# Performance work log

Hardware: AMD Instinct MI355X
Metric: run time of the kernel (lower is better)

The kernel has to match this reference:

```python
import jax, jax.numpy as jnp
import numpy as np

B = 8192       # atmospheric columns (batch)
NLAY = 60      # vertical levels (RNN sequence length)
NX = 4         # per-level input features
NXS = 3        # surface scalar inputs
NH1 = 64       # rnn1 hidden
NH2 = 64       # rnn2 hidden
NMEM = 16      # latent memory width (nh_mem)
NY = 4         # per-level outputs
NYS = 3        # surface outputs


def _lstm(x, h0, c0, Wih, Whh, bih, bhh):
    """PyTorch-convention LSTM (gate order i,f,g,o). x: [B,T,nx] -> ([B,T,nh], hL, cL)."""
    b = bih + bhh
    WihT = Wih.T
    WhhT = Whh.T

    def step(carry, xt):
        h, c = carry
        g = xt @ WihT + h @ WhhT + b
        i, f, gg, o = jnp.split(g, 4, axis=-1)
        c = jax.nn.sigmoid(f) * c + jax.nn.sigmoid(i) * jnp.tanh(gg)
        h = jax.nn.sigmoid(o) * jnp.tanh(c)
        return (h, c), h

    (hL, cL), ys = jax.lax.scan(step, (h0, c0), jnp.swapaxes(x, 0, 1))
    return jnp.swapaxes(ys, 0, 1), hL, cL


def setup_inputs() -> dict:
    key = jax.random.key(0)
    ks = jax.random.split(key, 30)

    def p(i, shape):
        return jax.random.normal(ks[i], shape, jnp.float32) * 0.05

    return {
        "inputs_main": jax.random.normal(ks[0], (B, NLAY, NX), jnp.float32),
        "inputs_aux": jax.random.normal(ks[1], (B, NXS), jnp.float32),
        "rnn1_mem": jax.random.normal(ks[2], (B, NLAY, NMEM), jnp.float32),
        # mlp_initial: Linear(nx, nneur[0])
        "Wi": p(3, (NH1, NX)), "bi": p(4, (NH1,)),
        # mlp_surface1/2: Linear(nx_sfc, nh_rnn1)
        "Ws1": p(5, (NH1, NXS)), "bs1": p(6, (NH1,)),
        "Ws2": p(7, (NH1, NXS)), "bs2": p(8, (NH1,)),
        # mlp_toa1/2: Linear(1, nh_rnn2)
        "Wt1": p(9, (NH2, 1)), "bt1": p(10, (NH2,)),
        "Wt2": p(11, (NH2, 1)), "bt2": p(12, (NH2,)),
        # rnn1: LSTM(NH1+NMEM -> NH1)
        "Wih1": p(13, (4 * NH1, NH1 + NMEM)), "Whh1": p(14, (4 * NH1, NH1)),
        "bih1": p(15, (4 * NH1,)), "bhh1": p(16, (4 * NH1,)),
        # rnn2: LSTM(NH1 -> NH2)
        "Wih2": p(17, (4 * NH2, NH1)), "Whh2": p(18, (4 * NH2, NH2)),
        "bih2": p(19, (4 * NH2,)), "bhh2": p(20, (4 * NH2,)),
        # mlp_latent: Linear(NH2, NMEM)
        "Wl": p(21, (NMEM, NH2)), "bl": p(22, (NMEM,)),
        # mlp_output: Linear(NMEM, NY)
        "Wo": p(23, (NY, NMEM)), "bo": p(24, (NY,)),
        # mlp_surface_output: Linear(NH2, NYS)
        "Wso": p(25, (NYS, NH2)), "bso": p(26, (NYS,)),
    }


def reference(inputs_main, inputs_aux, rnn1_mem, Wi, bi, Ws1, bs1, Ws2, bs2,
              Wt1, bt1, Wt2, bt2, Wih1, Whh1, bih1, bhh1, Wih2, Whh2, bih2, bhh2,
              Wl, bl, Wo, bo, Wso, bso):
    # initial MLP + tanh
    x = jnp.tanh(inputs_main @ Wi.T + bi)                       # [B,L,NH1]
    # concat convective memory
    x = jnp.concatenate([x, rnn1_mem], axis=2)                  # [B,L,NH1+NMEM]
    # rnn1 runs surface->TOA: flip level axis
    x = jnp.flip(x, axis=1)
    hx = jnp.tanh(inputs_aux @ Ws1.T + bs1)                     # surface-conditioned h0
    cx = jnp.tanh(inputs_aux @ Ws2.T + bs2)
    r1, _, _ = _lstm(x, hx, cx, Wih1, Whh1, bih1, bhh1)
    r1 = jnp.flip(r1, axis=1)                                   # back to TOA->surface
    # rnn2 initialized from TOA scalar
    toa = inputs_aux[:, 1:2]
    hx2 = toa @ Wt1.T + bt1
    cx2 = toa @ Wt2.T + bt2
    r2, hL, _ = _lstm(r1, hx2, cx2, Wih2, Whh2, bih2, bhh2)     # [B,L,NH2]
    # intermediate latent MLP -> new per-level memory
    lat = r2 @ Wl.T + bl                                        # [B,L,NMEM]
    new_mem = lat
    out = lat @ Wo.T + bo                                       # [B,L,NY]
    out_sfc = hL @ Wso.T + bso                                  # [B,NYS]
    return (out, out_sfc, new_mem)
```

## Files before the change

kernel.cpp:

```cpp
#include <hip/hip_runtime.h>
#include <hip/hip_bf16.h>

#define BATCH 8192
#define NLAY  60
#define ROWS  16
#define TPB   256
#define SX    136
#define SM    968
#define SI    244
#define LOG2E 1.44269504089f
#define T2L   2.88539008178f

typedef unsigned short ushort_t;
typedef __attribute__((ext_vector_type(8))) short short8;
typedef __attribute__((ext_vector_type(4))) float f32x4;
typedef __attribute__((ext_vector_type(4))) float f4v;

__device__ __forceinline__ float rcp_(float x) { return __builtin_amdgcn_rcpf(x); }
__device__ __forceinline__ float ex2_(float x) { return __builtin_amdgcn_exp2f(x); }
__device__ __forceinline__ ushort_t f2bu(float f) {
  unsigned u = __float_as_uint(f);
  return (ushort_t)((u + 0x7FFFu + ((u >> 16) & 1u)) >> 16);
}
__device__ __forceinline__ unsigned pkbf(float a, float b) {
  union { __hip_bfloat162 h; unsigned u; } c;
  c.h = __float22bfloat162_rn(make_float2(a, b));
  return c.u;
}
__device__ __forceinline__ f32x4 mfma16(short8 a, short8 b, f32x4 c) {
  return __builtin_amdgcn_mfma_f32_16x16x32_bf16(a, b, c, 0, 0, 0);
}

__global__ void wtranspose(const float* __restrict__ Wih1, const float* __restrict__ Whh1,
                           const float* __restrict__ Wih2, const float* __restrict__ Whh2,
                           const float* __restrict__ Wl,   const float* __restrict__ Wo,
                           const float* __restrict__ Wso,  ushort_t* __restrict__ frag) {
  int e = blockIdx.x * 256 + threadIdx.x;
  float v;
  if (e < 40960) {
    int j = e & 7, lx = (e >> 3) & 63, rest = e >> 9;
    int ks = rest % 5, gw = rest / 5;
    int g = gw & 3, wv = gw >> 2;
    int row = g * 64 + wv * 16 + (lx & 15);
    int k = ks * 32 + (lx >> 4) * 8 + j;
    v = (k < 64)  ? Wih1[row * 80 + k]
      : (k < 128) ? Whh1[row * 64 + (k - 64)]
      : (k < 144) ? Wih1[row * 80 + 64 + (k - 128)]
      : 0.0f;
    v *= (g == 2) ? T2L : LOG2E;
  } else if (e < 73728) {
    int e2 = e - 40960;
    int j = e2 & 7, lx = (e2 >> 3) & 63, rest = e2 >> 9;
    int ks = rest & 3, g = (rest >> 2) & 3, wv = rest >> 4;
    int row = g * 64 + wv * 16 + (lx & 15);
    int k = ks * 32 + (lx >> 4) * 8 + j;
    v = (k < 64) ? Wih2[row * 64 + k] : Whh2[row * 64 + (k - 64)];
    v *= (g == 2) ? T2L : LOG2E;
  } else if (e < 74752) {
    int e3 = e - 73728;
    int j = e3 & 7, lx = (e3 >> 3) & 63, ks = e3 >> 9;
    int n = lx & 15, k = ks * 32 + (lx >> 4) * 8 + j;
    v = Wl[n * 64 + k];
  } else if (e < 75776) {
    int e4 = e - 74752;
    int j = e4 & 7, lx = (e4 >> 3) & 63, ks = e4 >> 9;
    int n = lx & 15, k = ks * 32 + (lx >> 4) * 8 + j;
    v = 0.0f;
    if (n < 4) {
#pragma unroll
      for (int m = 0; m < 16; ++m) v += Wo[n * 16 + m] * Wl[m * 64 + k];
    }
  } else {
    int e5 = e - 75776;
    int j = e5 & 7, lx = (e5 >> 3) & 63, ks = e5 >> 9;
    int n = lx & 15, k = ks * 32 + (lx >> 4) * 8 + j;
    v = (n < 3) ? Wso[n * 64 + k] : 0.0f;
  }
  frag[e] = f2bu(v);
}

__global__ __launch_bounds__(TPB, 2)
void lstm_fused(const float* __restrict__ inputs_main, const float* __restrict__ inputs_aux,
                const float* __restrict__ rnn1_mem,
                const float* __restrict__ Wi,  const float* __restrict__ bi,
                const float* __restrict__ Ws1, const float* __restrict__ bs1,
                const float* __restrict__ Ws2, const float* __restrict__ bs2,
                const float* __restrict__ Wt1, const float* __restrict__ bt1,
                const float* __restrict__ Wt2, const float* __restrict__ bt2,
                const float* __restrict__ bih1, const float* __restrict__ bhh1,
                const float* __restrict__ bih2, const float* __restrict__ bhh2,
                const float* __restrict__ bl,  const float* __restrict__ Wo,
                const float* __restrict__ bo,  const float* __restrict__ bso,
                const ushort_t* __restrict__ frag,
                ushort_t* __restrict__ r1buf,
                float* __restrict__ out, float* __restrict__ out_sfc,
                float* __restrict__ new_mem) {
  const ushort_t* W1f = frag;
  const ushort_t* W2f = frag + 40960;
  const ushort_t* WlF = frag + 73728;
  const ushort_t* WcF = frag + 74752;
  const ushort_t* WsF = frag + 75776;

  __shared__ __align__(16) ushort_t xh[2][16 * SX];
  __shared__ __align__(16) ushort_t memAll[16 * SM];
  __shared__ __align__(16) float    inm[16 * SI];

  const int tid = threadIdx.x;
  const int lane = tid & 63, w = tid >> 6;
  const int ln = lane & 15, lq = lane >> 4;
  const int u = w * 16 + ln;
  const int rowbase = lq * 4;
  const int b0 = blockIdx.x * ROWS;
  const int xr = tid >> 4, xm = tid & 15, xc0 = xm * 4;
  const int rr8 = tid >> 3, ch8 = tid & 7;

  ushort_t* r1blk = r1buf + (size_t)blockIdx.x * (60 * 16 * 64);

  short8 B1f[4][5];
#pragma unroll
  for (int g = 0; g < 4; ++g)
#pragma unroll
    for (int ks = 0; ks < 5; ++ks)
      B1f[g][ks] = *(const short8*)(W1f + (((w * 4 + g) * 5 + ks) << 9) + (lane << 3));
  float bg1[4];
#pragma unroll
  for (int g = 0; g < 4; ++g)
    bg1[g] = (bih1[g * 64 + u] + bhh1[g * 64 + u]) * ((g == 2) ? T2L : LOG2E);

  f4v wif[4];
#pragma unroll
  for (int cc = 0; cc < 4; ++cc) wif[cc] = *(const f4v*)(Wi + (xc0 + cc) * 4) * T2L;
  f4v bifv = *(const f4v*)(bi + xc0) * T2L;

  for (int e = tid; e < 16 * 240; e += TPB) {
    int r = e / 240, c = e - r * 240;
    inm[r * SI + c] = inputs_main[(size_t)(b0 + r) * 240 + c];
  }
  for (int e = tid; e < 16 * 960; e += TPB) {
    int r = e / 960, c = e - r * 960;
    memAll[r * SM + c] = f2bu(rnn1_mem[(size_t)(b0 + r) * 960 + c]);
  }
  __syncthreads();

  float ct1[4];
  {
    f4v xin = *(const f4v*)&inm[xr * SI + 59 * 4];
    float xp[4];
#pragma unroll
    for (int cc = 0; cc < 4; ++cc) {
      float a = fmaf(wif[cc][3], xin[3], fmaf(wif[cc][2], xin[2],
                fmaf(wif[cc][1], xin[1], fmaf(wif[cc][0], xin[0], bifv[cc]))));
      xp[cc] = fmaf(rcp_(1.0f + ex2_(a)), -2.0f, 1.0f);
    }
    *(uint2*)&xh[0][xr * SX + xc0] = make_uint2(pkbf(xp[0], xp[1]), pkbf(xp[2], xp[3]));

    float w10 = Ws1[u * 3 + 0] * T2L, w11 = Ws1[u * 3 + 1] * T2L, w12 = Ws1[u * 3 + 2] * T2L;
    float bb1 = bs1[u] * T2L;
    float w20 = Ws2[u * 3 + 0] * T2L, w21 = Ws2[u * 3 + 1] * T2L, w22 = Ws2[u * 3 + 2] * T2L;
    float bb2 = bs2[u] * T2L;
#pragma unroll
    for (int reg = 0; reg < 4; ++reg) {
      int row = rowbase + reg;
      const float* ax = inputs_aux + (size_t)(b0 + row) * 3;
      float a0 = ax[0], a1 = ax[1], a2 = ax[2];
      float ha = w10 * a0 + w11 * a1 + w12 * a2 + bb1;
      xh[0][row * SX + 64 + u] = f2bu(fmaf(rcp_(1.0f + ex2_(ha)), -2.0f, 1.0f));
      float ca = w20 * a0 + w21 * a1 + w22 * a2 + bb2;
      ct1[reg] = fmaf(rcp_(1.0f + ex2_(ca)), -2.0f * T2L, T2L);
    }
  }
  __syncthreads();

  ushort_t* r1t = r1blk + rowbase * 64 + u;
  unsigned sxv[4], syv[4];
  int pb = 0;

  for (int tg = 14; tg >= 0; --tg) {
#pragma unroll
    for (int s = 3; s >= 0; --s) {
      const int t = tg * 4 + s;
      const int nb = pb ^ 1;
      const ushort_t* xrow = &xh[pb][ln * SX];
      short8 af0 = *(const short8*)(xrow + lq * 8);
      short8 af1 = *(const short8*)(xrow + 32 + lq * 8);
      short8 af2 = *(const short8*)(xrow + 64 + lq * 8);
      short8 af3 = *(const short8*)(xrow + 96 + lq * 8);
      short8 af4 = {};
      if (lq < 2) af4 = *(const short8*)(memAll + ln * SM + t * 16 + lq * 8);

      f32x4 acc[4];
#pragma unroll
      for (int g = 0; g < 4; ++g) acc[g] = (f32x4){bg1[g], bg1[g], bg1[g], bg1[g]};
#pragma unroll
      for (int g = 0; g < 4; ++g) {
        acc[g] = mfma16(af0, B1f[g][0], acc[g]);
        acc[g] = mfma16(af1, B1f[g][1], acc[g]);
        acc[g] = mfma16(af2, B1f[g][2], acc[g]);
        acc[g] = mfma16(af3, B1f[g][3], acc[g]);
        acc[g] = mfma16(af4, B1f[g][4], acc[g]);
      }

      if (t > 0) {
        f4v xin = *(const f4v*)&inm[xr * SI + (t - 1) * 4];
        float xp[4];
#pragma unroll
        for (int cc = 0; cc < 4; ++cc) {
          float a = fmaf(wif[cc][3], xin[3], fmaf(wif[cc][2], xin[2],
                    fmaf(wif[cc][1], xin[1], fmaf(wif[cc][0], xin[0], bifv[cc]))));
          xp[cc] = fmaf(rcp_(1.0f + ex2_(a)), -2.0f, 1.0f);
        }
        *(uint2*)&xh[nb][xr * SX + xc0] = make_uint2(pkbf(xp[0], xp[1]), pkbf(xp[2], xp[3]));
      }

      float h[4];
#pragma unroll
      for (int reg = 0; reg < 4; ++reg) {
        float si = rcp_(1.0f + ex2_(-acc[0][reg]));
        float sf = rcp_(1.0f + ex2_(-acc[1][reg]));
        float so = rcp_(1.0f + ex2_(-acc[3][reg]));
        float gt = fmaf(rcp_(1.0f + ex2_(acc[2][reg])), -2.0f * T2L, T2L);
        ct1[reg] = fmaf(sf, ct1[reg], si * gt);
        float tc = fmaf(rcp_(1.0f + ex2_(ct1[reg])), -2.0f, 1.0f);
        h[reg] = so * tc;
      }
      unsigned h01 = pkbf(h[0], h[1]), h23 = pkbf(h[2], h[3]);
      sxv[s] = h01; syv[s] = h23;
      if (t > 0) {
        xh[nb][(rowbase + 0) * SX + 64 + u] = (ushort_t)h01;
        xh[nb][(rowbase + 1) * SX + 64 + u] = (ushort_t)(h01 >> 16);
        xh[nb][(rowbase + 2) * SX + 64 + u] = (ushort_t)h23;
        xh[nb][(rowbase + 3) * SX + 64 + u] = (ushort_t)(h23 >> 16);
      } else {
        xh[nb][(rowbase + 0) * SX + u] = (ushort_t)h01;
        xh[nb][(rowbase + 1) * SX + u] = (ushort_t)(h01 >> 16);
        xh[nb][(rowbase + 2) * SX + u] = (ushort_t)h23;
        xh[nb][(rowbase + 3) * SX + u] = (ushort_t)(h23 >> 16);
      }
      __syncthreads();
      pb = nb;
    }
    ushort_t* rp = r1t + (tg << 12);
#pragma unroll
    for (int s = 0; s < 4; ++s) {
      unsigned a = sxv[s], b = syv[s];
      rp[s * 1024 + 0 * 64] = (ushort_t)a;
      rp[s * 1024 + 1 * 64] = (ushort_t)(a >> 16);
      rp[s * 1024 + 2 * 64] = (ushort_t)b;
      rp[s * 1024 + 3 * 64] = (ushort_t)(b >> 16);
    }
  }

  short8 B2f[4][4];
#pragma unroll
  for (int g = 0; g < 4; ++g)
#pragma unroll
    for (int ks = 0; ks < 4; ++ks)
      B2f[g][ks] = *(const short8*)(W2f + (((w * 4 + g) * 4 + ks) << 9) + (lane << 3));
  float bg2[4];
#pragma unroll
  for (int g = 0; g < 4; ++g)
    bg2[g] = (bih2[g * 64 + u] + bhh2[g * 64 + u]) * ((g == 2) ? T2L : LOG2E);

  float ct2[4];
  {
    float wt1u = Wt1[u], wt2u = Wt2[u], bt1u = bt1[u], bt2u = bt2[u];
#pragma unroll
    for (int reg = 0; reg < 4; ++reg) {
      int row = rowbase + reg;
      float toa = inputs_aux[(size_t)(b0 + row) * 3 + 1];
      xh[pb][row * SX + 64 + u] = f2bu(toa * wt1u + bt1u);
      ct2[reg] = (toa * wt2u + bt2u) * T2L;
    }
  }
  short8 PW0 = {}, PW1 = {};
  float pbias = 0.0f;
  if (w == 0) {
    PW0 = *(const short8*)(WlF + (lane << 3));
    PW1 = *(const short8*)(WlF + 512 + (lane << 3));
    pbias = bl[ln];
  } else if (w == 1) {
    PW0 = *(const short8*)(WcF + (lane << 3));
    PW1 = *(const short8*)(WcF + 512 + (lane << 3));
    if (ln < 4) {
      float a = bo[ln];
#pragma unroll
      for (int m = 0; m < 16; ++m) a += Wo[ln * 16 + m] * bl[m];
      pbias = a;
    }
  } else if (w == 2) {
    PW0 = *(const short8*)(WsF + (lane << 3));
    PW1 = *(const short8*)(WsF + 512 + (lane << 3));
    pbias = (ln < 3) ? bso[ln] : 0.0f;
  }
  const ushort_t* r1rp = r1blk + 1024 + rr8 * 64 + ch8 * 8;
  float* nmb = new_mem + (size_t)(b0 + rowbase) * 960 + ln;
  float* outb = out + (size_t)(b0 + rowbase) * 240 + ln;
  f32x4 pst[4];
  __syncthreads();

  for (int tg = 0; tg < 15; ++tg) {
#pragma unroll
    for (int s = 0; s < 4; ++s) {
      const int t = tg * 4 + s;
      const int nb = pb ^ 1;
      short8 r1v = {};
      if (t < 59 && tid < 128) r1v = *(const short8*)(r1rp + t * 1024);

      const ushort_t* xrow = &xh[pb][ln * SX];
      short8 af0 = *(const short8*)(xrow + lq * 8);
      short8 af1 = *(const short8*)(xrow + 32 + lq * 8);
      short8 af2 = *(const short8*)(xrow + 64 + lq * 8);
      short8 af3 = *(const short8*)(xrow + 96 + lq * 8);

      f32x4 acc[4];
#pragma unroll
      for (int g = 0; g < 4; ++g) acc[g] = (f32x4){bg2[g], bg2[g], bg2[g], bg2[g]};
#pragma unroll
      for (int g = 0; g < 4; ++g) {
        acc[g] = mfma16(af0, B2f[g][0], acc[g]);
        acc[g] = mfma16(af1, B2f[g][1], acc[g]);
        acc[g] = mfma16(af2, B2f[g][2], acc[g]);
        acc[g] = mfma16(af3, B2f[g][3], acc[g]);
      }

      if (t > 0 && w < 2) {
        f32x4 ap = (f32x4){pbias, pbias, pbias, pbias};
        ap = mfma16(af2, PW0, ap);
        ap = mfma16(af3, PW1, ap);
        pst[(t - 1) & 3] = ap;
      }

      float h[4];
#pragma unroll
      for (int reg = 0; reg < 4; ++reg) {
        float si = rcp_(1.0f + ex2_(-acc[0][reg]));
        float sf = rcp_(1.0f + ex2_(-acc[1][reg]));
        float so = rcp_(1.0f + ex2_(-acc[3][reg]));
        float gt = fmaf(rcp_(1.0f + ex2_(acc[2][reg])), -2.0f * T2L, T2L);
        ct2[reg] = fmaf(sf, ct2[reg], si * gt);
        float tc = fmaf(rcp_(1.0f + ex2_(ct2[reg])), -2.0f, 1.0f);
        h[reg] = so * tc;
      }
      unsigned h01 = pkbf(h[0], h[1]), h23 = pkbf(h[2], h[3]);
      xh[nb][(rowbase + 0) * SX + 64 + u] = (ushort_t)h01;
      xh[nb][(rowbase + 1) * SX + 64 + u] = (ushort_t)(h01 >> 16);
      xh[nb][(rowbase + 2) * SX + 64 + u] = (ushort_t)h23;
      xh[nb][(rowbase + 3) * SX + 64 + u] = (ushort_t)(h23 >> 16);
      if (t < 59 && tid < 128)
        *(short8*)&xh[nb][rr8 * SX + ch8 * 8] = r1v;
      __syncthreads();
      pb = nb;
    }
    if (w < 2) {
      const int base = tg * 4;
#pragma unroll
      for (int k = 0; k < 4; ++k) {
        const int pt = (k == 3) ? base - 1 : base + k;
        if (pt < 0) continue;
        f32x4 ap = pst[k];
        if (w == 0) {
#pragma unroll
          for (int reg = 0; reg < 4; ++reg) nmb[reg * 960 + pt * 16] = ap[reg];
        } else if (ln < 4) {
#pragma unroll
          for (int reg = 0; reg < 4; ++reg) outb[reg * 240 + pt * 4] = ap[reg];
        }
      }
    }
  }

  if (w < 3) {
    const ushort_t* xrow = &xh[pb][ln * SX];
    short8 aL0 = *(const short8*)(xrow + 64 + lq * 8);
    short8 aL1 = *(const short8*)(xrow + 96 + lq * 8);
    f32x4 ap = (f32x4){pbias, pbias, pbias, pbias};
    ap = mfma16(aL0, PW0, ap);
    ap = mfma16(aL1, PW1, ap);
    if (w == 0) {
#pragma unroll
      for (int reg = 0; reg < 4; ++reg) nmb[reg * 960 + 59 * 16] = ap[reg];
    } else if (w == 1) {
      if (ln < 4) {
#pragma unroll
        for (int reg = 0; reg < 4; ++reg) outb[reg * 240 + 59 * 4] = ap[reg];
      }
    } else {
      if (ln < 3) {
#pragma unroll
        for (int reg = 0; reg < 4; ++reg)
          out_sfc[(size_t)(b0 + rowbase + reg) * 3 + ln] = ap[reg];
      }
    }
  }
}

extern "C" void kernel_launch(void* const* d_in, const int* in_sizes, int n_in,
                              void* d_out, int out_size, void* d_ws, size_t ws_size,
                              hipStream_t stream) {
  (void)in_sizes; (void)n_in; (void)out_size; (void)ws_size;
  const float* inputs_main = (const float*)d_in[0];
  const float* inputs_aux  = (const float*)d_in[1];
  const float* rnn1_mem    = (const float*)d_in[2];
  const float* Wi   = (const float*)d_in[3];
  const float* bi   = (const float*)d_in[4];
  const float* Ws1  = (const float*)d_in[5];
  const float* bs1  = (const float*)d_in[6];
  const float* Ws2  = (const float*)d_in[7];
  const float* bs2  = (const float*)d_in[8];
  const float* Wt1  = (const float*)d_in[9];
  const float* bt1  = (const float*)d_in[10];
  const float* Wt2  = (const float*)d_in[11];
  const float* bt2  = (const float*)d_in[12];
  const float* Wih1 = (const float*)d_in[13];
  const float* Whh1 = (const float*)d_in[14];
  const float* bih1 = (const float*)d_in[15];
  const float* bhh1 = (const float*)d_in[16];
  const float* Wih2 = (const float*)d_in[17];
  const float* Whh2 = (const float*)d_in[18];
  const float* bih2 = (const float*)d_in[19];
  const float* bhh2 = (const float*)d_in[20];
  const float* Wl   = (const float*)d_in[21];
  const float* bl   = (const float*)d_in[22];
  const float* Wo   = (const float*)d_in[23];
  const float* bo   = (const float*)d_in[24];
  const float* Wso  = (const float*)d_in[25];
  const float* bso  = (const float*)d_in[26];

  float* out     = (float*)d_out;
  float* out_sfc = out + (size_t)BATCH * NLAY * 4;
  float* new_mem = out_sfc + (size_t)BATCH * 3;

  ushort_t* frag  = (ushort_t*)d_ws;
  ushort_t* r1buf = (ushort_t*)((char*)d_ws + 153600);

  wtranspose<<<300, 256, 0, stream>>>(Wih1, Whh1, Wih2, Whh2, Wl, Wo, Wso, frag);
  lstm_fused<<<BATCH / ROWS, TPB, 0, stream>>>(
      inputs_main, inputs_aux, rnn1_mem, Wi, bi, Ws1, bs1, Ws2, bs2,
      Wt1, bt1, Wt2, bt2, bih1, bhh1, bih2, bhh2, bl, Wo, bo, bso,
      frag, r1buf, out, out_sfc, new_mem);
}
```

Before: 255.9 us.

## Halve rows per block, split gate math across lane halves, stream memory input

Each block now handles 8 batch rows instead of 16, which doubles the block count and raises launch bounds to four blocks per CU. The 16-row MFMA tiles are kept with zero padding, so half the matrix work is wasted. Accumulator rows are redistributed across lane halves with permlane32 swaps, so each lane evaluates the gate nonlinearities for two rows instead of four. The full rnn1_mem tile is no longer staged in LDS; a double-buffered per-4-step slice is prefetched from global memory. Together these cut LDS use and per-thread work to allow more concurrent waves, in exchange for redundant MFMA work and extra cross-lane moves.

After: 556.5 us. +117.5%, slower.

```diff
diff --git a/kernel.cpp b/kernel.cpp
--- a/kernel.cpp
+++ b/kernel.cpp
@@ -3,10 +3,10 @@
 
 #define BATCH 8192
 #define NLAY  60
-#define ROWS  16
+#define ROWS  8
 #define TPB   256
 #define SX    136
-#define SM    968
+#define SMG   72
 #define SI    244
 #define LOG2E 1.44269504089f
 #define T2L   2.88539008178f
@@ -15,6 +15,7 @@
 typedef __attribute__((ext_vector_type(8))) short short8;
 typedef __attribute__((ext_vector_type(4))) float f32x4;
 typedef __attribute__((ext_vector_type(4))) float f4v;
+typedef __attribute__((ext_vector_type(2))) unsigned u32x2;
 
 __device__ __forceinline__ float rcp_(float x) { return __builtin_amdgcn_rcpf(x); }
 __device__ __forceinline__ float ex2_(float x) { return __builtin_amdgcn_exp2f(x); }
@@ -29,6 +30,16 @@
 }
 __device__ __forceinline__ f32x4 mfma16(short8 a, short8 b, f32x4 c) {
   return __builtin_amdgcn_mfma_f32_16x16x32_bf16(a, b, c, 0, 0, 0);
+}
+__device__ __forceinline__ float lsplit(float lo, float hi) {
+#if __has_builtin(__builtin_amdgcn_permlane32_swap)
+  u32x2 r = __builtin_amdgcn_permlane32_swap(__float_as_uint(lo), __float_as_uint(hi),
+                                             false, false);
+  return __uint_as_float(r[0]);
+#else
+  float h2 = __shfl_xor(hi, 32, 64);
+  return (threadIdx.x & 32) ? h2 : lo;
+#endif
 }
 
 __global__ void wtranspose(const float* __restrict__ Wih1, const float* __restrict__ Whh1,
@@ -79,7 +90,7 @@
   frag[e] = f2bu(v);
 }
 
-__global__ __launch_bounds__(TPB, 2)
+__global__ __launch_bounds__(TPB, 4)
 void lstm_fused(const float* __restrict__ inputs_main, const float* __restrict__ inputs_aux,
                 const float* __restrict__ rnn1_mem,
                 const float* __restrict__ Wi,  const float* __restrict__ bi,
@@ -102,19 +113,20 @@
   const ushort_t* WsF = frag + 75776;
 
   __shared__ __align__(16) ushort_t xh[2][16 * SX];
-  __shared__ __align__(16) ushort_t memAll[16 * SM];
-  __shared__ __align__(16) float    inm[16 * SI];
+  __shared__ __align__(16) ushort_t memG[2][8 * SMG];
+  __shared__ __align__(16) float    inm[8 * SI];
 
   const int tid = threadIdx.x;
   const int lane = tid & 63, w = tid >> 6;
   const int ln = lane & 15, lq = lane >> 4;
   const int u = w * 16 + ln;
-  const int rowbase = lq * 4;
+  const int hr0 = (lane < 32) ? (lq * 4) : ((lq - 2) * 4 + 2);
+  const int rowbase = (lq < 2) ? lq * 4 : 0;
   const int b0 = blockIdx.x * ROWS;
-  const int xr = tid >> 4, xm = tid & 15, xc0 = xm * 4;
-  const int rr8 = tid >> 3, ch8 = tid & 7;
-
-  ushort_t* r1blk = r1buf + (size_t)blockIdx.x * (60 * 16 * 64);
+  const int xr = tid >> 5, xc0 = (tid & 31) * 2;
+  const int mr = tid >> 4, mc0 = (tid & 15) * 4;
+
+  ushort_t* r1blk = r1buf + (size_t)blockIdx.x * (60 * 8 * 64);
 
   short8 B1f[4][5];
 #pragma unroll
@@ -127,55 +139,61 @@
   for (int g = 0; g < 4; ++g)
     bg1[g] = (bih1[g * 64 + u] + bhh1[g * 64 + u]) * ((g == 2) ? T2L : LOG2E);
 
-  f4v wif[4];
-#pragma unroll
-  for (int cc = 0; cc < 4; ++cc) wif[cc] = *(const f4v*)(Wi + (xc0 + cc) * 4) * T2L;
-  f4v bifv = *(const f4v*)(bi + xc0) * T2L;
-
-  for (int e = tid; e < 16 * 240; e += TPB) {
+  f4v wif0 = *(const f4v*)(Wi + (xc0 + 0) * 4) * T2L;
+  f4v wif1 = *(const f4v*)(Wi + (xc0 + 1) * 4) * T2L;
+  float bif0 = bi[xc0] * T2L, bif1 = bi[xc0 + 1] * T2L;
+
+  {
+    unsigned* xz = (unsigned*)&xh[0][0];
+    for (int e = tid; e < 16 * SX; e += TPB) xz[e] = 0;
+  }
+  for (int e = tid; e < 8 * 240; e += TPB) {
     int r = e / 240, c = e - r * 240;
     inm[r * SI + c] = inputs_main[(size_t)(b0 + r) * 240 + c];
   }
-  for (int e = tid; e < 16 * 960; e += TPB) {
-    int r = e / 960, c = e - r * 960;
-    memAll[r * SM + c] = f2bu(rnn1_mem[(size_t)(b0 + r) * 960 + c]);
+  if (tid < 128) {
+    f4v mv = *(const f4v*)(rnn1_mem + (size_t)(b0 + mr) * 960 + 14 * 64 + mc0);
+    *(uint2*)&memG[0][mr * SMG + mc0] =
+        make_uint2(pkbf(mv[0], mv[1]), pkbf(mv[2], mv[3]));
   }
   __syncthreads();
 
-  float ct1[4];
+  float ct1[2];
   {
     f4v xin = *(const f4v*)&inm[xr * SI + 59 * 4];
-    float xp[4];
-#pragma unroll
-    for (int cc = 0; cc < 4; ++cc) {
-      float a = fmaf(wif[cc][3], xin[3], fmaf(wif[cc][2], xin[2],
-                fmaf(wif[cc][1], xin[1], fmaf(wif[cc][0], xin[0], bifv[cc]))));
-      xp[cc] = fmaf(rcp_(1.0f + ex2_(a)), -2.0f, 1.0f);
-    }
-    *(uint2*)&xh[0][xr * SX + xc0] = make_uint2(pkbf(xp[0], xp[1]), pkbf(xp[2], xp[3]));
+    float a0 = fmaf(wif0[3], xin[3], fmaf(wif0[2], xin[2],
+               fmaf(wif0[1], xin[1], fmaf(wif0[0], xin[0], bif0))));
+    float a1 = fmaf(wif1[3], xin[3], fmaf(wif1[2], xin[2],
+               fmaf(wif1[1], xin[1], fmaf(wif1[0], xin[0], bif1))));
+    float xp0 = fmaf(rcp_(1.0f + ex2_(a0)), -2.0f, 1.0f);
+    float xp1 = fmaf(rcp_(1.0f + ex2_(a1)), -2.0f, 1.0f);
+    *(unsigned*)&xh[0][xr * SX + xc0] = pkbf(xp0, xp1);
 
     float w10 = Ws1[u * 3 + 0] * T2L, w11 = Ws1[u * 3 + 1] * T2L, w12 = Ws1[u * 3 + 2] * T2L;
     float bb1 = bs1[u] * T2L;
     float w20 = Ws2[u * 3 + 0] * T2L, w21 = Ws2[u * 3 + 1] * T2L, w22 = Ws2[u * 3 + 2] * T2L;
     float bb2 = bs2[u] * T2L;
 #pragma unroll
-    for (int reg = 0; reg < 4; ++reg) {
-      int row = rowbase + reg;
+    for (int p = 0; p < 2; ++p) {
+      int row = hr0 + p;
       const float* ax = inputs_aux + (size_t)(b0 + row) * 3;
-      float a0 = ax[0], a1 = ax[1], a2 = ax[2];
-      float ha = w10 * a0 + w11 * a1 + w12 * a2 + bb1;
+      float A0 = ax[0], A1 = ax[1], A2 = ax[2];
+      float ha = w10 * A0 + w11 * A1 + w12 * A2 + bb1;
       xh[0][row * SX + 64 + u] = f2bu(fmaf(rcp_(1.0f + ex2_(ha)), -2.0f, 1.0f));
-      float ca = w20 * a0 + w21 * a1 + w22 * a2 + bb2;
-      ct1[reg] = fmaf(rcp_(1.0f + ex2_(ca)), -2.0f * T2L, T2L);
+      float ca = w20 * A0 + w21 * A1 + w22 * A2 + bb2;
+      ct1[p] = fmaf(rcp_(1.0f + ex2_(ca)), -2.0f * T2L, T2L);
     }
   }
   __syncthreads();
 
-  ushort_t* r1t = r1blk + rowbase * 64 + u;
-  unsigned sxv[4], syv[4];
+  unsigned sxv[4];
   int pb = 0;
 
   for (int tg = 14; tg >= 0; --tg) {
+    f4v mpre;
+    const bool stg = (tg > 0) && (tid < 128);
+    if (stg)
+      mpre = *(const f4v*)(rnn1_mem + (size_t)(b0 + mr) * 960 + (tg - 1) * 64 + mc0);
 #pragma unroll
     for (int s = 3; s >= 0; --s) {
       const int t = tg * 4 + s;
@@ -186,7 +204,8 @@
       short8 af2 = *(const short8*)(xrow + 64 + lq * 8);
       short8 af3 = *(const short8*)(xrow + 96 + lq * 8);
       short8 af4 = {};
-      if (lq < 2) af4 = *(const short8*)(memAll + ln * SM + t * 16 + lq * 8);
+      if (lq < 2 && ln < 8)
+        af4 = *(const short8*)(&memG[tg & 1][ln * SMG + s * 16 + lq * 8]);
 
       f32x4 acc[4];
 #pragma unroll
@@ -202,51 +221,58 @@
 
       if (t > 0) {
         f4v xin = *(const f4v*)&inm[xr * SI + (t - 1) * 4];
-        float xp[4];
-#pragma unroll
-        for (int cc = 0; cc < 4; ++cc) {
-          float a = fmaf(wif[cc][3], xin[3], fmaf(wif[cc][2], xin[2],
-                    fmaf(wif[cc][1], xin[1], fmaf(wif[cc][0], xin[0], bifv[cc]))));
-          xp[cc] = fmaf(rcp_(1.0f + ex2_(a)), -2.0f, 1.0f);
+        float a0 = fmaf(wif0[3], xin[3], fmaf(wif0[2], xin[2],
+                   fmaf(wif0[1], xin[1], fmaf(wif0[0], xin[0], bif0))));
+        float a1 = fmaf(wif1[3], xin[3], fmaf(wif1[2], xin[2],
+                   fmaf(wif1[1], xin[1], fmaf(wif1[0], xin[0], bif1))));
+        float xp0 = fmaf(rcp_(1.0f + ex2_(a0)), -2.0f, 1.0f);
+        float xp1 = fmaf(rcp_(1.0f + ex2_(a1)), -2.0f, 1.0f);
+        *(unsigned*)&xh[nb][xr * SX + xc0] = pkbf(xp0, xp1);
+      }
+      if (s == 2 && stg) {
+        *(uint2*)&memG[(tg - 1) & 1][mr * SMG + mc0] =
+            make_uint2(pkbf(mpre[0], mpre[1]), pkbf(mpre[2], mpre[3]));
+      }
+
+      float h0, h1;
+      {
+        float e0[4], e1[4];
+#pragma unroll
+        for (int g = 0; g < 4; ++g) {
+          e0[g] = lsplit(acc[g][0], acc[g][2]);
+          e1[g] = lsplit(acc[g][1], acc[g][3]);
         }
-        *(uint2*)&xh[nb][xr * SX + xc0] = make_uint2(pkbf(xp[0], xp[1]), pkbf(xp[2], xp[3]));
-      }
-
-      float h[4];
-#pragma unroll
-      for (int reg = 0; reg < 4; ++reg) {
-        float si = rcp_(1.0f + ex2_(-acc[0][reg]));
-        float sf = rcp_(1.0f + ex2_(-acc[1][reg]));
-        float so = rcp_(1.0f + ex2_(-acc[3][reg]));
-        float gt = fmaf(rcp_(1.0f + ex2_(acc[2][reg])), -2.0f * T2L, T2L);
-        ct1[reg] = fmaf(sf, ct1[reg], si * gt);
-        float tc = fmaf(rcp_(1.0f + ex2_(ct1[reg])), -2.0f, 1.0f);
-        h[reg] = so * tc;
-      }
-      unsigned h01 = pkbf(h[0], h[1]), h23 = pkbf(h[2], h[3]);
-      sxv[s] = h01; syv[s] = h23;
+        float si = rcp_(1.0f + ex2_(-e0[0]));
+        float sf = rcp_(1.0f + ex2_(-e0[1]));
+        float so = rcp_(1.0f + ex2_(-e0[3]));
+        float gt = fmaf(rcp_(1.0f + ex2_(e0[2])), -2.0f * T2L, T2L);
+        ct1[0] = fmaf(sf, ct1[0], si * gt);
+        h0 = so * fmaf(rcp_(1.0f + ex2_(ct1[0])), -2.0f, 1.0f);
+        si = rcp_(1.0f + ex2_(-e1[0]));
+        sf = rcp_(1.0f + ex2_(-e1[1]));
+        so = rcp_(1.0f + ex2_(-e1[3]));
+        gt = fmaf(rcp_(1.0f + ex2_(e1[2])), -2.0f * T2L, T2L);
+        ct1[1] = fmaf(sf, ct1[1], si * gt);
+        h1 = so * fmaf(rcp_(1.0f + ex2_(ct1[1])), -2.0f, 1.0f);
+      }
+      unsigned h01 = pkbf(h0, h1);
+      sxv[s] = h01;
       if (t > 0) {
-        xh[nb][(rowbase + 0) * SX + 64 + u] = (ushort_t)h01;
-        xh[nb][(rowbase + 1) * SX + 64 + u] = (ushort_t)(h01 >> 16);
-        xh[nb][(rowbase + 2) * SX + 64 + u] = (ushort_t)h23;
-        xh[nb][(rowbase + 3) * SX + 64 + u] = (ushort_t)(h23 >> 16);
+        xh[nb][(hr0 + 0) * SX + 64 + u] = (ushort_t)h01;
+        xh[nb][(hr0 + 1) * SX + 64 + u] = (ushort_t)(h01 >> 16);
       } else {
-        xh[nb][(rowbase + 0) * SX + u] = (ushort_t)h01;
-        xh[nb][(rowbase + 1) * SX + u] = (ushort_t)(h01 >> 16);
-        xh[nb][(rowbase + 2) * SX + u] = (ushort_t)h23;
-        xh[nb][(rowbase + 3) * SX + u] = (ushort_t)(h23 >> 16);
+        xh[nb][(hr0 + 0) * SX + u] = (ushort_t)h01;
+        xh[nb][(hr0 + 1) * SX + u] = (ushort_t)(h01 >> 16);
       }
       __syncthreads();
       pb = nb;
     }
-    ushort_t* rp = r1t + (tg << 12);
+    ushort_t* rp = r1blk + ((size_t)(tg * 4) * 512) + hr0 * 64 + u;
 #pragma unroll
     for (int s = 0; s < 4; ++s) {
-      unsigned a = sxv[s], b = syv[s];
-      rp[s * 1024 + 0 * 64] = (ushort_t)a;
-      rp[s * 1024 + 1 * 64] = (ushort_t)(a >> 16);
-      rp[s * 1024 + 2 * 64] = (ushort_t)b;
-      rp[s * 1024 + 3 * 64] = (ushort_t)(b >> 16);
+      unsigned a = sxv[s];
+      rp[s * 512] = (ushort_t)a;
+      rp[s * 512 + 64] = (ushort_t)(a >> 16);
     }
   }
 
@@ -261,15 +287,15 @@
   for (int g = 0; g < 4; ++g)
     bg2[g] = (bih2[g * 64 + u] + bhh2[g * 64 + u]) * ((g == 2) ? T2L : LOG2E);
 
-  float ct2[4];
+  float ct2[2];
   {
     float wt1u = Wt1[u], wt2u = Wt2[u], bt1u = bt1[u], bt2u = bt2[u];
 #pragma unroll
-    for (int reg = 0; reg < 4; ++reg) {
-      int row = rowbase + reg;
+    for (int p = 0; p < 2; ++p) {
+      int row = hr0 + p;
       float toa = inputs_aux[(size_t)(b0 + row) * 3 + 1];
       xh[pb][row * SX + 64 + u] = f2bu(toa * wt1u + bt1u);
-      ct2[reg] = (toa * wt2u + bt2u) * T2L;
+      ct2[p] = (toa * wt2u + bt2u) * T2L;
     }
   }
   short8 PW0 = {}, PW1 = {};
@@ -292,7 +318,7 @@
     PW1 = *(const short8*)(WsF + 512 + (lane << 3));
     pbias = (ln < 3) ? bso[ln] : 0.0f;
   }
-  const ushort_t* r1rp = r1blk + 1024 + rr8 * 64 + ch8 * 8;
+  const ushort_t* r1rp = r1blk + 512 + mr * 64 + mc0;
   float* nmb = new_mem + (size_t)(b0 + rowbase) * 960 + ln;
   float* outb = out + (size_t)(b0 + rowbase) * 240 + ln;
   f32x4 pst[4];
@@ -303,8 +329,9 @@
     for (int s = 0; s < 4; ++s) {
       const int t = tg * 4 + s;
       const int nb = pb ^ 1;
-      short8 r1v = {};
-      if (t < 59 && tid < 128) r1v = *(const short8*)(r1rp + t * 1024);
+      uint2 r1v;
+      const bool lr1 = (t < 59) && (tid < 128);
+      if (lr1) r1v = *(const uint2*)(r1rp + t * 512);
 
       const ushort_t* xrow = &xh[pb][ln * SX];
       short8 af0 = *(const short8*)(xrow + lq * 8);
@@ -330,28 +357,35 @@
         pst[(t - 1) & 3] = ap;
       }
 
-      float h[4];
-#pragma unroll
-      for (int reg = 0; reg < 4; ++reg) {
-        float si = rcp_(1.0f + ex2_(-acc[0][reg]));
-        float sf = rcp_(1.0f + ex2_(-acc[1][reg]));
-        float so = rcp_(1.0f + ex2_(-acc[3][reg]));
-        float gt = fmaf(rcp_(1.0f + ex2_(acc[2][reg])), -2.0f * T2L, T2L);
-        ct2[reg] = fmaf(sf, ct2[reg], si * gt);
-        float tc = fmaf(rcp_(1.0f + ex2_(ct2[reg])), -2.0f, 1.0f);
-        h[reg] = so * tc;
-      }
-      unsigned h01 = pkbf(h[0], h[1]), h23 = pkbf(h[2], h[3]);
-      xh[nb][(rowbase + 0) * SX + 64 + u] = (ushort_t)h01;
-      xh[nb][(rowbase + 1) * SX + 64 + u] = (ushort_t)(h01 >> 16);
-      xh[nb][(rowbase + 2) * SX + 64 + u] = (ushort_t)h23;
-      xh[nb][(rowbase + 3) * SX + 64 + u] = (ushort_t)(h23 >> 16);
-      if (t < 59 && tid < 128)
-        *(short8*)&xh[nb][rr8 * SX + ch8 * 8] = r1v;
+      float h0, h1;
+      {
+        float e0[4], e1[4];
+#pragma unroll
+        for (int g = 0; g < 4; ++g) {
+          e0[g] = lsplit(acc[g][0], acc[g][2]);
+          e1[g] = lsplit(acc[g][1], acc[g][3]);
+        }
+        float si = rcp_(1.0f + ex2_(-e0[0]));
+        float sf = rcp_(1.0f + ex2_(-e0[1]));
+        float so = rcp_(1.0f + ex2_(-e0[3]));
+        float gt = fmaf(rcp_(1.0f + ex2_(e0[2])), -2.0f * T2L, T2L);
+        ct2[0] = fmaf(sf, ct2[0], si * gt);
+        h0 = so * fmaf(rcp_(1.0f + ex2_(ct2[0])), -2.0f, 1.0f);
+        si = rcp_(1.0f + ex2_(-e1[0]));
+        sf = rcp_(1.0f + ex2_(-e1[1]));
+        so = rcp_(1.0f + ex2_(-e1[3]));
+        gt = fmaf(rcp_(1.0f + ex2_(e1[2])), -2.0f * T2L, T2L);
+        ct2[1] = fmaf(sf, ct2[1], si * gt);
+        h1 = so * fmaf(rcp_(1.0f + ex2_(ct2[1])), -2.0f, 1.0f);
+      }
+      unsigned h01 = pkbf(h0, h1);
+      xh[nb][(hr0 + 0) * SX + 64 + u] = (ushort_t)h01;
+      xh[nb][(hr0 + 1) * SX + 64 + u] = (ushort_t)(h01 >> 16);
+      if (lr1) *(uint2*)&xh[nb][mr * SX + mc0] = r1v;
       __syncthreads();
       pb = nb;
     }
-    if (w < 2) {
+    if (w < 2 && lq < 2) {
       const int base = tg * 4;
 #pragma unroll
       for (int k = 0; k < 4; ++k) {
@@ -376,19 +410,21 @@
     f32x4 ap = (f32x4){pbias, pbias, pbias, pbias};
     ap = mfma16(aL0, PW0, ap);
     ap = mfma16(aL1, PW1, ap);
-    if (w == 0) {
-#pragma unroll
-      for (int reg = 0; reg < 4; ++reg) nmb[reg * 960 + 59 * 16] = ap[reg];
-    } else if (w == 1) {
-      if (ln < 4) {
-#pragma unroll
-        for (int reg = 0; reg < 4; ++reg) outb[reg * 240 + 59 * 4] = ap[reg];
-      }
-    } else {
-      if (ln < 3) {
-#pragma unroll
-        for (int reg = 0; reg < 4; ++reg)
-          out_sfc[(size_t)(b0 + rowbase + reg) * 3 + ln] = ap[reg];
+    if (lq < 2) {
+      if (w == 0) {
+#pragma unroll
+        for (int reg = 0; reg < 4; ++reg) nmb[reg * 960 + 59 * 16] = ap[reg];
+      } else if (w == 1) {
+        if (ln < 4) {
+#pragma unroll
+          for (int reg = 0; reg < 4; ++reg) outb[reg * 240 + 59 * 4] = ap[reg];
+        }
+      } else {
+        if (ln < 3) {
+#pragma unroll
+          for (int reg = 0; reg < 4; ++reg)
+            out_sfc[(size_t)(b0 + rowbase + reg) * 3 + ln] = ap[reg];
+        }
       }
     }
   }
```
